# Kernel optimization log

Measured on AMD Instinct MI355X. Metric: run time of the kernel, lower is better.

Reference implementation:

```python
import jax, jax.numpy as jnp
import numpy as np

SEQ, BATCH, IN_DIM, HID, NQ = 256, 512, 512, 512, 32


def setup_inputs() -> dict:
    key = jax.random.key(0)
    k_in, k_fw, k_fb, k_ow, k_ob = jax.random.split(key, 5)
    s_fc = 1.0 / np.sqrt(IN_DIM + HID)
    s_out = 1.0 / np.sqrt(NQ)
    return {
        "inputs": jax.random.normal(k_in, (SEQ, BATCH, IN_DIM), dtype=jnp.float32),
        "fc_w": jax.random.uniform(k_fw, (NQ, IN_DIM + HID), jnp.float32, -s_fc, s_fc),
        "fc_b": jax.random.uniform(k_fb, (NQ,), jnp.float32, -s_fc, s_fc),
        "out_w": jax.random.uniform(k_ow, (HID, NQ), jnp.float32, -s_out, s_out),
        "out_b": jax.random.uniform(k_ob, (HID,), jnp.float32, -s_out, s_out),
    }


def _quantum_gate(q_in):
    # RX(x_i) on wire i then CNOT ladder; <Z_k> = prod_{j<=k} cos(x_j)
    return jnp.cumprod(jnp.cos(q_in), axis=-1)


def reference(inputs, fc_w, fc_b, out_w, out_b):
    batch = inputs.shape[1]
    h0 = jnp.zeros((batch, HID), dtype=inputs.dtype)
    c0 = jnp.zeros((batch, HID), dtype=inputs.dtype)

    def step(carry, x):
        hx, cx = carry
        combined = jnp.concatenate([x, hx], axis=1)            # [B, IN+HID]
        q_in = combined @ fc_w.T + fc_b                        # [B, NQ]
        q = _quantum_gate(q_in)                                # [B, NQ]
        f = jax.nn.sigmoid(q) @ out_w.T + out_b                # [B, HID]
        i = f                                                  # same circuit & weights as f
        g = jnp.tanh(q) @ out_w.T + out_b
        o = f                                                  # same as f
        cx = f * cx + i * g
        hx = o * jnp.tanh(cx)
        return (hx, cx), hx

    (hx, cx), outputs = jax.lax.scan(step, (h0, c0), inputs)
    return outputs, hx, cx
```

## Files before the change

### kernel.cpp

```cpp
#include <hip/hip_runtime.h>
#include <math.h>

#define SEQ 256
#define BATCH 512
#define IN_DIM 512
#define HID 512
#define NQ 32

typedef float v2f __attribute__((ext_vector_type(2)));

__device__ __forceinline__ float fast_rcp(float x) { return __builtin_amdgcn_rcpf(x); }

__device__ __forceinline__ float tanh_fast(float x) {
    float a = fabsf(x);
    float e = __expf(-2.0f * a);
    float r = (1.0f - e) * fast_rcp(1.0f + e);
    return copysignf(r, x);
}

template <int CTRL>
__device__ __forceinline__ float dpp_add(float x) {
    int t = __builtin_amdgcn_update_dpp(0, __float_as_int(x), CTRL, 0xF, 0xF, false);
    return x + __int_as_float(t);
}
__device__ __forceinline__ float reduce16_add(float x) {
    x = dpp_add<0xB1>(x);
    x = dpp_add<0x4E>(x);
    x = dpp_add<0x141>(x);
    x = dpp_add<0x140>(x);
    return x;
}
__device__ __forceinline__ float reduce4_add(float x) {
    x = dpp_add<0xB1>(x);
    x = dpp_add<0x4E>(x);
    return x;
}
template <int CTRL, int ROW_MASK>
__device__ __forceinline__ float dpp_mul1(float x) {
    int t = __builtin_amdgcn_update_dpp(0x3f800000 , __float_as_int(x),
                                        CTRL, ROW_MASK, 0xF, false);
    return x * __int_as_float(t);
}
__device__ __forceinline__ float scan32_mul(float x) {
    x = dpp_mul1<0x111, 0xF>(x);
    x = dpp_mul1<0x112, 0xF>(x);
    x = dpp_mul1<0x114, 0xF>(x);
    x = dpp_mul1<0x118, 0xF>(x);
    x = dpp_mul1<0x142, 0xA>(x);
    return x;
}

#define BLOCK_BARRIER_LDS() asm volatile("s_waitcnt lgkmcnt(0)\n\ts_barrier" ::: "memory")
#define WAVE_FENCE_LDS()                                        \
    do {                                                        \
        asm volatile("s_waitcnt lgkmcnt(0)" ::: "memory");      \
        __builtin_amdgcn_sched_barrier(0);                      \
    } while (0)

__global__ __launch_bounds__(256, 4) void xp_kernel(const float* __restrict__ x,
                                                    const float* __restrict__ fc_w,
                                                    const float* __restrict__ fc_b,
                                                    float* __restrict__ xp) {
    const int tid = threadIdx.x;
    const int g2 = tid >> 4;
    const int s  = tid & 15;

    __shared__ float4 tile4[16 * 128];

    v2f wA_lo[8], wA_hi[8], wB_lo[8], wB_hi[8];
    {
        const float* wrA = fc_w + (size_t)(g2 * 2 + 0) * (IN_DIM + HID) + 4 * s;
        const float* wrB = fc_w + (size_t)(g2 * 2 + 1) * (IN_DIM + HID) + 4 * s;
#pragma unroll
        for (int j = 0; j < 8; ++j) {
            float4 a = *reinterpret_cast<const float4*>(wrA + 64 * j);
            float4 b = *reinterpret_cast<const float4*>(wrB + 64 * j);
            wA_lo[j] = (v2f){a.x, a.y}; wA_hi[j] = (v2f){a.z, a.w};
            wB_lo[j] = (v2f){b.x, b.y}; wB_hi[j] = (v2f){b.z, b.w};
        }
    }
    const float2 bias2 = reinterpret_cast<const float2*>(fc_b)[g2];

    const float4* x4 = reinterpret_cast<const float4*>(x) + (size_t)blockIdx.x * (16 * 128);
#pragma unroll
    for (int q = 0; q < 8; ++q)
        tile4[tid + 256 * q] = x4[tid + 256 * q];
    __syncthreads();

    const int row0 = blockIdx.x * 16;
    float2* xp2 = reinterpret_cast<float2*>(xp);
    for (int rp = 0; rp < 8; ++rp) {
        const int r0 = 2 * rp, r1 = 2 * rp + 1;
        v2f aA0 = (v2f){0.f, 0.f}, aA1 = aA0, aB0 = aA0, aB1 = aA0;
        v2f bA0 = aA0, bA1 = aA0, bB0 = aA0, bB1 = aA0;
#pragma unroll
        for (int j = 0; j < 8; j += 2) {
            float4 h0 = tile4[r0 * 128 + s + 16 * j];
            float4 h1 = tile4[r1 * 128 + s + 16 * j];
            v2f h0lo = (v2f){h0.x, h0.y}, h0hi = (v2f){h0.z, h0.w};
            v2f h1lo = (v2f){h1.x, h1.y}, h1hi = (v2f){h1.z, h1.w};
            aA0 = __builtin_elementwise_fma(h0lo, wA_lo[j], aA0);
            aA0 = __builtin_elementwise_fma(h0hi, wA_hi[j], aA0);
            aA1 = __builtin_elementwise_fma(h0lo, wB_lo[j], aA1);
            aA1 = __builtin_elementwise_fma(h0hi, wB_hi[j], aA1);
            aB0 = __builtin_elementwise_fma(h1lo, wA_lo[j], aB0);
            aB0 = __builtin_elementwise_fma(h1hi, wA_hi[j], aB0);
            aB1 = __builtin_elementwise_fma(h1lo, wB_lo[j], aB1);
            aB1 = __builtin_elementwise_fma(h1hi, wB_hi[j], aB1);
            float4 g0 = tile4[r0 * 128 + s + 16 * (j + 1)];
            float4 g1 = tile4[r1 * 128 + s + 16 * (j + 1)];
            v2f g0lo = (v2f){g0.x, g0.y}, g0hi = (v2f){g0.z, g0.w};
            v2f g1lo = (v2f){g1.x, g1.y}, g1hi = (v2f){g1.z, g1.w};
            bA0 = __builtin_elementwise_fma(g0lo, wA_lo[j + 1], bA0);
            bA0 = __builtin_elementwise_fma(g0hi, wA_hi[j + 1], bA0);
            bA1 = __builtin_elementwise_fma(g0lo, wB_lo[j + 1], bA1);
            bA1 = __builtin_elementwise_fma(g0hi, wB_hi[j + 1], bA1);
            bB0 = __builtin_elementwise_fma(g1lo, wA_lo[j + 1], bB0);
            bB0 = __builtin_elementwise_fma(g1hi, wA_hi[j + 1], bB0);
            bB1 = __builtin_elementwise_fma(g1lo, wB_lo[j + 1], bB1);
            bB1 = __builtin_elementwise_fma(g1hi, wB_hi[j + 1], bB1);
        }
        v2f sA0 = aA0 + bA0, sA1 = aA1 + bA1, sB0 = aB0 + bB0, sB1 = aB1 + bB1;
        float rA0 = reduce16_add(sA0.x + sA0.y);
        float rA1 = reduce16_add(sA1.x + sA1.y);
        float rB0 = reduce16_add(sB0.x + sB0.y);
        float rB1 = reduce16_add(sB1.x + sB1.y);
        if (s == 0) {
            xp2[(size_t)(row0 + r0) * 16 + g2] = make_float2(rA0 + bias2.x, rA1 + bias2.y);
            xp2[(size_t)(row0 + r1) * 16 + g2] = make_float2(rB0 + bias2.x, rB1 + bias2.y);
        }
    }
}

__global__ __launch_bounds__(256, 2) void rnn_kernel(const float* __restrict__ xp,
                                                     const float* __restrict__ fc_w,
                                                     const float* __restrict__ out_w,
                                                     const float* __restrict__ out_b,
                                                     float* __restrict__ out) {
    const int b = blockIdx.x;
    const int tid = threadIdx.x;
    const int w4 = tid >> 6;
    const int lane = tid & 63;
    const int l31 = lane & 31;
    const int grp = lane >> 2;
    const int sl = lane & 3;

    __shared__ __align__(16) float hbuf[HID];
    __shared__ __align__(16) float pbuf[2][4][NQ];
    __shared__ __align__(16) float wbuf[4][64];
    __shared__ __align__(16) float xps[SEQ * NQ];

    v2f whA_lo[8], whA_hi[8], whB_lo[8], whB_hi[8];
    {
        const int kbase = IN_DIM + 128 * w4 + 32 * sl;
        const float* wrA = fc_w + (size_t)(grp * 2 + 0) * (IN_DIM + HID) + kbase;
        const float* wrB = fc_w + (size_t)(grp * 2 + 1) * (IN_DIM + HID) + kbase;
#pragma unroll
        for (int j = 0; j < 8; ++j) {
            float4 a = *reinterpret_cast<const float4*>(wrA + 4 * j);
            float4 c = *reinterpret_cast<const float4*>(wrB + 4 * j);
            whA_lo[j] = (v2f){a.x, a.y}; whA_hi[j] = (v2f){a.z, a.w};
            whB_lo[j] = (v2f){c.x, c.y}; whB_hi[j] = (v2f){c.z, c.w};
        }
    }
    const int hid0 = 128 * w4 + lane;
    const int hid1 = hid0 + 64;
    float ow0[NQ], ow1[NQ];
    {
        const float4* o0 = reinterpret_cast<const float4*>(out_w + (size_t)hid0 * NQ);
        const float4* o1 = reinterpret_cast<const float4*>(out_w + (size_t)hid1 * NQ);
#pragma unroll
        for (int q4 = 0; q4 < 8; ++q4) {
            float4 a = o0[q4], bq = o1[q4];
            ow0[4 * q4 + 0] = a.x;  ow0[4 * q4 + 1] = a.y;
            ow0[4 * q4 + 2] = a.z;  ow0[4 * q4 + 3] = a.w;
            ow1[4 * q4 + 0] = bq.x; ow1[4 * q4 + 1] = bq.y;
            ow1[4 * q4 + 2] = bq.z; ow1[4 * q4 + 3] = bq.w;
        }
    }
    const float ob0 = out_b[hid0];
    const float ob1 = out_b[hid1];

    {
        const float4* xpg = reinterpret_cast<const float4*>(xp);
        float4* xps4 = reinterpret_cast<float4*>(xps);
#pragma unroll
        for (int k = 0; k < 8; ++k) {
            int idx = tid + 256 * k;
            int t = idx >> 3, q4 = idx & 7;
            xps4[idx] = xpg[((size_t)t * BATCH + b) * 8 + q4];
        }
    }
    hbuf[tid] = 0.0f;
    hbuf[tid + 256] = 0.0f;
    float c0 = 0.0f, c1 = 0.0f;
    __syncthreads();

    float* hx_out = out + (size_t)SEQ * BATCH * HID + (size_t)b * HID;
    float* cx_out = hx_out + (size_t)BATCH * HID;

    const float4* h4 = reinterpret_cast<const float4*>(hbuf) + (32 * w4 + 8 * sl);

    int par = 0;
    for (int t = 0; t < SEQ; ++t) {
        v2f aA = (v2f){0.f, 0.f}, aB = aA, bA = aA, bB = aA;
#pragma unroll
        for (int j = 0; j < 8; j += 2) {
            float4 hv = h4[j];
            v2f hlo = (v2f){hv.x, hv.y}, hhi = (v2f){hv.z, hv.w};
            aA = __builtin_elementwise_fma(hlo, whA_lo[j], aA);
            aA = __builtin_elementwise_fma(hhi, whA_hi[j], aA);
            aB = __builtin_elementwise_fma(hlo, whB_lo[j], aB);
            aB = __builtin_elementwise_fma(hhi, whB_hi[j], aB);
            float4 gv = h4[j + 1];
            v2f glo = (v2f){gv.x, gv.y}, ghi = (v2f){gv.z, gv.w};
            bA = __builtin_elementwise_fma(glo, whA_lo[j + 1], bA);
            bA = __builtin_elementwise_fma(ghi, whA_hi[j + 1], bA);
            bB = __builtin_elementwise_fma(glo, whB_lo[j + 1], bB);
            bB = __builtin_elementwise_fma(ghi, whB_hi[j + 1], bB);
        }
        v2f sA = aA + bA, sB = aB + bB;
        float rA = reduce4_add(sA.x + sA.y);
        float rB = reduce4_add(sB.x + sB.y);
        if (sl == 0)
            *reinterpret_cast<float2*>(&pbuf[par][w4][2 * grp]) = make_float2(rA, rB);

        BLOCK_BARRIER_LDS();

        {
            const float* pb = &pbuf[par][0][0];
            float qin = (pb[l31] + pb[32 + l31]) + (pb[64 + l31] + pb[96 + l31])
                      + xps[t * NQ + l31];
            float pp = scan32_mul(__cosf(qin));
            float arg = (lane < 32) ? -pp : (-2.0f * pp);
            float e = __expf(arg);
            float num = (lane < 32) ? 1.0f : (1.0f - e);
            float val = num * fast_rcp(1.0f + e);
            wbuf[w4][(l31 << 1) | (lane >> 5)] = val;
        }
        WAVE_FENCE_LDS();

        const float4* st4 = reinterpret_cast<const float4*>(wbuf[w4]);
        v2f a0 = (v2f){ob0, ob0};
        v2f a1 = (v2f){ob1, ob1};
#pragma unroll
        for (int m = 0; m < 16; ++m) {
            float4 v = st4[m];
            v2f plo = (v2f){v.x, v.y}, phi = (v2f){v.z, v.w};
            a0 = __builtin_elementwise_fma(plo, (v2f){ow0[2 * m], ow0[2 * m]}, a0);
            a0 = __builtin_elementwise_fma(phi, (v2f){ow0[2 * m + 1], ow0[2 * m + 1]}, a0);
            a1 = __builtin_elementwise_fma(plo, (v2f){ow1[2 * m], ow1[2 * m]}, a1);
            a1 = __builtin_elementwise_fma(phi, (v2f){ow1[2 * m + 1], ow1[2 * m + 1]}, a1);
        }
        float f0 = a0.x, g0 = a0.y, f1 = a1.x, g1 = a1.y;
        c0 = f0 * (c0 + g0);
        c1 = f1 * (c1 + g1);
        float h0 = f0 * tanh_fast(c0);
        float h1 = f1 * tanh_fast(c1);

        hbuf[hid0] = h0;
        hbuf[hid1] = h1;
        float* orow = out + ((size_t)t * BATCH + b) * HID;
        orow[hid0] = h0;
        orow[hid1] = h1;
        if (t == SEQ - 1) {
            hx_out[hid0] = h0; hx_out[hid1] = h1;
            cx_out[hid0] = c0; cx_out[hid1] = c1;
        }
        WAVE_FENCE_LDS();
        par ^= 1;
    }
}

extern "C" void kernel_launch(void* const* d_in, const int* in_sizes, int n_in,
                              void* d_out, int out_size, void* d_ws, size_t ws_size,
                              hipStream_t stream) {
    const float* inputs = (const float*)d_in[0];
    const float* fc_w   = (const float*)d_in[1];
    const float* fc_b   = (const float*)d_in[2];
    const float* out_w  = (const float*)d_in[3];
    const float* out_b  = (const float*)d_in[4];
    float* out = (float*)d_out;
    float* xp  = (float*)d_ws;

    xp_kernel<<<(SEQ * BATCH) / 16, 256, 0, stream>>>(inputs, fc_w, fc_b, xp);
    rnn_kernel<<<BATCH, 256, 0, stream>>>(xp, fc_w, out_w, out_b, out);
}
```

Baseline: 369.7 us.

## Interleave hidden-state reads, repack output matvec, drop wave fences

Recurrent weights are now loaded with an interleaved stride, so the four sub-lanes of each group read adjacent float4 chunks of the hidden state instead of chunks spread far apart. This is meant to cut LDS bank conflicts. The output projection now keeps the sigmoid and tanh values in separate contiguous halves of a per-wave buffer and uses packed FMAs against paired out_w values, with more independent accumulators. The explicit per-wave LDS wait/sched barriers are removed, leaving intra-wave ordering to the hardware and compiler. The launch bound is also expressed as waves_per_eu(2,2). Correctness now depends on in-order LDS access within a wave.

```diff
diff --git a/kernel.cpp b/kernel.cpp
--- a/kernel.cpp
+++ b/kernel.cpp
@@ -51,11 +51,6 @@
 }
 
 #define BLOCK_BARRIER_LDS() asm volatile("s_waitcnt lgkmcnt(0)\n\ts_barrier" ::: "memory")
-#define WAVE_FENCE_LDS()                                        \
-    do {                                                        \
-        asm volatile("s_waitcnt lgkmcnt(0)" ::: "memory");      \
-        __builtin_amdgcn_sched_barrier(0);                      \
-    } while (0)
 
 __global__ __launch_bounds__(256, 4) void xp_kernel(const float* __restrict__ x,
                                                     const float* __restrict__ fc_w,
@@ -132,11 +127,13 @@
     }
 }
 
-__global__ __launch_bounds__(256, 2) void rnn_kernel(const float* __restrict__ xp,
-                                                     const float* __restrict__ fc_w,
-                                                     const float* __restrict__ out_w,
-                                                     const float* __restrict__ out_b,
-                                                     float* __restrict__ out) {
+__global__ __launch_bounds__(256)
+__attribute__((amdgpu_waves_per_eu(2, 2)))
+void rnn_kernel(const float* __restrict__ xp,
+                const float* __restrict__ fc_w,
+                const float* __restrict__ out_w,
+                const float* __restrict__ out_b,
+                float* __restrict__ out) {
     const int b = blockIdx.x;
     const int tid = threadIdx.x;
     const int w4 = tid >> 6;
@@ -147,35 +144,35 @@
 
     __shared__ __align__(16) float hbuf[HID];
     __shared__ __align__(16) float pbuf[2][4][NQ];
-    __shared__ __align__(16) float wbuf[4][64];
+    __shared__ __align__(16) float pwbuf[4][64];
     __shared__ __align__(16) float xps[SEQ * NQ];
 
     v2f whA_lo[8], whA_hi[8], whB_lo[8], whB_hi[8];
     {
-        const int kbase = IN_DIM + 128 * w4 + 32 * sl;
+        const int kbase = IN_DIM + 128 * w4 + 4 * sl;
         const float* wrA = fc_w + (size_t)(grp * 2 + 0) * (IN_DIM + HID) + kbase;
         const float* wrB = fc_w + (size_t)(grp * 2 + 1) * (IN_DIM + HID) + kbase;
 #pragma unroll
         for (int j = 0; j < 8; ++j) {
-            float4 a = *reinterpret_cast<const float4*>(wrA + 4 * j);
-            float4 c = *reinterpret_cast<const float4*>(wrB + 4 * j);
+            float4 a = *reinterpret_cast<const float4*>(wrA + 16 * j);
+            float4 c = *reinterpret_cast<const float4*>(wrB + 16 * j);
             whA_lo[j] = (v2f){a.x, a.y}; whA_hi[j] = (v2f){a.z, a.w};
             whB_lo[j] = (v2f){c.x, c.y}; whB_hi[j] = (v2f){c.z, c.w};
         }
     }
     const int hid0 = 128 * w4 + lane;
     const int hid1 = hid0 + 64;
-    float ow0[NQ], ow1[NQ];
+    v2f ow0v[16], ow1v[16];
     {
         const float4* o0 = reinterpret_cast<const float4*>(out_w + (size_t)hid0 * NQ);
         const float4* o1 = reinterpret_cast<const float4*>(out_w + (size_t)hid1 * NQ);
 #pragma unroll
         for (int q4 = 0; q4 < 8; ++q4) {
             float4 a = o0[q4], bq = o1[q4];
-            ow0[4 * q4 + 0] = a.x;  ow0[4 * q4 + 1] = a.y;
-            ow0[4 * q4 + 2] = a.z;  ow0[4 * q4 + 3] = a.w;
-            ow1[4 * q4 + 0] = bq.x; ow1[4 * q4 + 1] = bq.y;
-            ow1[4 * q4 + 2] = bq.z; ow1[4 * q4 + 3] = bq.w;
+            ow0v[2 * q4 + 0] = (v2f){a.x, a.y};
+            ow0v[2 * q4 + 1] = (v2f){a.z, a.w};
+            ow1v[2 * q4 + 0] = (v2f){bq.x, bq.y};
+            ow1v[2 * q4 + 1] = (v2f){bq.z, bq.w};
         }
     }
     const float ob0 = out_b[hid0];
@@ -199,20 +196,20 @@
     float* hx_out = out + (size_t)SEQ * BATCH * HID + (size_t)b * HID;
     float* cx_out = hx_out + (size_t)BATCH * HID;
 
-    const float4* h4 = reinterpret_cast<const float4*>(hbuf) + (32 * w4 + 8 * sl);
+    const float4* h4s = reinterpret_cast<const float4*>(hbuf) + (32 * w4 + sl);
 
     int par = 0;
     for (int t = 0; t < SEQ; ++t) {
         v2f aA = (v2f){0.f, 0.f}, aB = aA, bA = aA, bB = aA;
 #pragma unroll
         for (int j = 0; j < 8; j += 2) {
-            float4 hv = h4[j];
+            float4 hv = h4s[4 * j];
             v2f hlo = (v2f){hv.x, hv.y}, hhi = (v2f){hv.z, hv.w};
             aA = __builtin_elementwise_fma(hlo, whA_lo[j], aA);
             aA = __builtin_elementwise_fma(hhi, whA_hi[j], aA);
             aB = __builtin_elementwise_fma(hlo, whB_lo[j], aB);
             aB = __builtin_elementwise_fma(hhi, whB_hi[j], aB);
-            float4 gv = h4[j + 1];
+            float4 gv = h4s[4 * (j + 1)];
             v2f glo = (v2f){gv.x, gv.y}, ghi = (v2f){gv.z, gv.w};
             bA = __builtin_elementwise_fma(glo, whA_lo[j + 1], bA);
             bA = __builtin_elementwise_fma(ghi, whA_hi[j + 1], bA);
@@ -236,23 +233,31 @@
             float e = __expf(arg);
             float num = (lane < 32) ? 1.0f : (1.0f - e);
             float val = num * fast_rcp(1.0f + e);
-            wbuf[w4][(l31 << 1) | (lane >> 5)] = val;
-        }
-        WAVE_FENCE_LDS();
-
-        const float4* st4 = reinterpret_cast<const float4*>(wbuf[w4]);
-        v2f a0 = (v2f){ob0, ob0};
-        v2f a1 = (v2f){ob1, ob1};
-#pragma unroll
-        for (int m = 0; m < 16; ++m) {
-            float4 v = st4[m];
-            v2f plo = (v2f){v.x, v.y}, phi = (v2f){v.z, v.w};
-            a0 = __builtin_elementwise_fma(plo, (v2f){ow0[2 * m], ow0[2 * m]}, a0);
-            a0 = __builtin_elementwise_fma(phi, (v2f){ow0[2 * m + 1], ow0[2 * m + 1]}, a0);
-            a1 = __builtin_elementwise_fma(plo, (v2f){ow1[2 * m], ow1[2 * m]}, a1);
-            a1 = __builtin_elementwise_fma(phi, (v2f){ow1[2 * m + 1], ow1[2 * m + 1]}, a1);
-        }
-        float f0 = a0.x, g0 = a0.y, f1 = a1.x, g1 = a1.y;
+            pwbuf[w4][lane] = val;
+        }
+
+        const float4* sb4 = reinterpret_cast<const float4*>(&pwbuf[w4][0]);
+        const float4* tb4 = sb4 + 8;
+        v2f f0a = (v2f){0.f, 0.f}, f0b = f0a, g0a = f0a, g0b = f0a;
+        v2f f1a = f0a, f1b = f0a, g1a = f0a, g1b = f0a;
+#pragma unroll
+        for (int m = 0; m < 8; ++m) {
+            float4 sv = sb4[m];
+            float4 tv = tb4[m];
+            v2f slo = (v2f){sv.x, sv.y}, shi = (v2f){sv.z, sv.w};
+            v2f tlo = (v2f){tv.x, tv.y}, thi = (v2f){tv.z, tv.w};
+            f0a = __builtin_elementwise_fma(slo, ow0v[2 * m + 0], f0a);
+            f0b = __builtin_elementwise_fma(shi, ow0v[2 * m + 1], f0b);
+            g0a = __builtin_elementwise_fma(tlo, ow0v[2 * m + 0], g0a);
+            g0b = __builtin_elementwise_fma(thi, ow0v[2 * m + 1], g0b);
+            f1a = __builtin_elementwise_fma(slo, ow1v[2 * m + 0], f1a);
+            f1b = __builtin_elementwise_fma(shi, ow1v[2 * m + 1], f1b);
+            g1a = __builtin_elementwise_fma(tlo, ow1v[2 * m + 0], g1a);
+            g1b = __builtin_elementwise_fma(thi, ow1v[2 * m + 1], g1b);
+        }
+        v2f sf0 = f0a + f0b, sg0 = g0a + g0b, sf1 = f1a + f1b, sg1 = g1a + g1b;
+        float f0 = ob0 + sf0.x + sf0.y, g0 = ob0 + sg0.x + sg0.y;
+        float f1 = ob1 + sf1.x + sf1.y, g1 = ob1 + sg1.x + sg1.y;
         c0 = f0 * (c0 + g0);
         c1 = f1 * (c1 + g1);
         float h0 = f0 * tanh_fast(c0);
@@ -267,7 +272,6 @@
             hx_out[hid0] = h0; hx_out[hid1] = h1;
             cx_out[hid0] = c0; cx_out[hid1] = c1;
         }
-        WAVE_FENCE_LDS();
         par ^= 1;
     }
 }
```

Measured after the change: 365.8 us, median of 2. About the same (-1.0%).
